# Performance work log

Measured on AMD Instinct MI355X. Metric: run time of the kernel, lower is better.

The kernel has to match this reference:

```python
import jax, jax.numpy as jnp
import numpy as np

N_NODES = 327680      # 8192 graphs * 40 nodes/graph
N_EDGES = 2621440     # avg degree 8
NODES_PER_GRAPH = 40


def _lin(k, fan_in, fan_out):
    s = 1.0 / np.sqrt(fan_in)
    return jax.random.uniform(k, (fan_in, fan_out), jnp.float32, -s, s)


def setup_inputs() -> dict:
    key = jax.random.key(0)
    ks = jax.random.split(key, 12)
    x = jax.random.normal(ks[0], (N_NODES, 58), jnp.float32)
    edge_index = jax.random.randint(ks[1], (2, N_EDGES), 0, N_NODES, dtype=jnp.int32)
    return {
        "x": x,
        "edge_index": edge_index,
        "W1": _lin(ks[2], 58, 96),  "b1": jnp.zeros((96,), jnp.float32),
        "W2": _lin(ks[3], 96, 48),  "b2": jnp.zeros((48,), jnp.float32),
        "l1_w": _lin(ks[4], 40 * 48, 256), "l1_b": jnp.zeros((256,), jnp.float32),
        "l2_w": _lin(ks[5], 256, 64),      "l2_b": jnp.zeros((64,), jnp.float32),
        "l3_w": _lin(ks[6], 64, 1),        "l3_b": jnp.zeros((1,), jnp.float32),
    }


def gcn_conv(x, src, dst, W, b, n):
    # PyG GCNConv: h = X W; out[i] = sum_{(j->i)} d_j^-1/2 d_i^-1/2 h[j] + b
    h = x @ W                                   # [N, out]
    deg = jnp.zeros((n,), h.dtype).at[dst].add(1.0)
    dinv = jnp.where(deg > 0, jax.lax.rsqrt(deg), 0.0)
    norm = dinv[src] * dinv[dst]                # [E]
    out = jax.ops.segment_sum(h[src] * norm[:, None], dst, num_segments=n)
    return out + b


def reference(x, edge_index, W1, b1, W2, b2, l1_w, l1_b, l2_w, l2_b, l3_w, l3_b):
    n = x.shape[0]
    loop = jnp.arange(n, dtype=edge_index.dtype)        # self-loops (PyG default)
    src = jnp.concatenate([edge_index[0], loop])
    dst = jnp.concatenate([edge_index[1], loop])
    h = jax.nn.relu(gcn_conv(x, src, dst, W1, b1, n))   # dropout is identity in eval
    h = jax.nn.relu(gcn_conv(h, src, dst, W2, b2, n))
    g = h.reshape(n // NODES_PER_GRAPH, NODES_PER_GRAPH * 48)
    g = jax.nn.relu(g @ l1_w + l1_b)
    g = jax.nn.relu(g @ l2_w + l2_b)
    return jax.nn.sigmoid(g @ l3_w + l3_b)              # [B, 1]
```

## Files before the change

### kernel.cpp

```cpp
#include <hip/hip_runtime.h>

#define N_NODES 327680
#define N_EDGES 2621440
#define NGRAPH  8192
#define NB      640
#define BCAPE   4608

typedef unsigned int uint;
typedef unsigned short u16;
typedef __attribute__((ext_vector_type(8))) short s16x8;
typedef __attribute__((ext_vector_type(4))) float f32x4;

__device__ __forceinline__ float b2f(u16 h){ return __uint_as_float(((uint)h)<<16); }
__device__ __forceinline__ u16 f2b(float f){
    uint u = __float_as_uint(f);
    u += 0x7fffu + ((u>>16)&1u);
    return (u16)(u>>16);
}


__global__ void k_initgcur(int* __restrict__ gcur){
    int i = blockIdx.x*256 + threadIdx.x;
    if (i < NB) gcur[i] = i*BCAPE;
}


__global__ __launch_bounds__(256) void k_partition(
    const int* __restrict__ src, const int* __restrict__ dst,
    int* __restrict__ gcur, uint2* __restrict__ staging)
{
    __shared__ int cnt[NB], base_[NB];
    int tid = threadIdx.x;
    for (int i = tid; i < NB; i += 256) cnt[i] = 0;
    __syncthreads();
    int e0 = blockIdx.x*4096;
    int d[16];
    #pragma unroll
    for (int j = 0; j < 16; ++j){
        d[j] = dst[e0 + j*256 + tid];
        atomicAdd(&cnt[d[j] >> 9], 1);
    }
    __syncthreads();
    for (int i = tid; i < NB; i += 256)
        base_[i] = atomicAdd(&gcur[i], cnt[i]);
    __syncthreads();
    for (int i = tid; i < NB; i += 256) cnt[i] = 0;
    __syncthreads();
    #pragma unroll
    for (int j = 0; j < 16; ++j){
        int e = e0 + j*256 + tid;
        int b = d[j] >> 9;
        int r = atomicAdd(&cnt[b], 1);
        staging[base_[b] + r] = make_uint2((uint)src[e], (uint)d[j]);
    }
}


__global__ __launch_bounds__(512) void k_bucket(
    const uint2* __restrict__ staging, const int* __restrict__ gcur,
    int* __restrict__ rowst, int* __restrict__ rendg, float* __restrict__ dinvg,
    int* __restrict__ csr, int* __restrict__ perm)
{
    __shared__ uint2 sedge[BCAPE];
    __shared__ int deg[512];
    __shared__ int sc[512];
    __shared__ int cur[512];
    __shared__ int dh[64], dbase[64];
    const int b = blockIdx.x;
    const int tid = threadIdx.x;
    const int lo = b*BCAPE;
    int cnt = gcur[b] - lo;
    if (cnt > BCAPE) cnt = BCAPE;
    deg[tid] = 0;
    if (tid < 64) dh[tid] = 0;
    __syncthreads();
    for (int t = tid; t < cnt; t += 512){
        uint2 ed = staging[lo + t];
        sedge[t] = ed;
        atomicAdd(&deg[ed.y & 511], 1);
    }
    __syncthreads();
    int d = deg[tid];
    sc[tid] = d;
    __syncthreads();
    for (int o = 1; o < 512; o <<= 1){
        int v = (tid >= o) ? sc[tid-o] : 0;
        __syncthreads();
        sc[tid] += v;
        __syncthreads();
    }
    int incl = sc[tid];
    int excl = incl - d;
    int gnode = b*512 + tid;
    rowst[gnode] = lo + excl;
    rendg[gnode] = lo + incl;
    dinvg[gnode] = 1.0f / sqrtf((float)(d + 1));
    cur[tid] = lo + excl;
    int bin = min(d, 63);
    atomicAdd(&dh[bin], 1);
    __syncthreads();
    if (tid == 0){
        int a = 0;
        #pragma unroll
        for (int i = 0; i < 64; ++i){ dbase[i] = a; a += dh[i]; dh[i] = 0; }
    }
    __syncthreads();
    int pos = dbase[bin] + atomicAdd(&dh[bin], 1);
    perm[b*512 + pos] = gnode;
    for (int t = tid; t < cnt; t += 512){
        uint2 ed = sedge[t];
        int p = atomicAdd(&cur[ed.y & 511], 1);
        csr[p] = (int)ed.x;
    }
}


__global__ __launch_bounds__(256) void k_trconv(const float* __restrict__ in, u16* __restrict__ out,
                                                int K, int N, int Kpad){
    __shared__ u16 t[64][72];
    int kb = blockIdx.x*64, nb = blockIdx.y*64;
    for (int i = threadIdx.x; i < 4096; i += 256){
        int k = i >> 6, n = i & 63;
        int gk = kb + k, gn = nb + n;
        float v = (gk < K && gn < N) ? in[(size_t)gk*N + gn] : 0.f;
        t[n][k] = f2b(v);
    }
    __syncthreads();
    for (int i = threadIdx.x; i < 4096; i += 256){
        int n = i >> 6, k = i & 63;
        int gk = kb + k, gn = nb + n;
        if (gn < N && gk < Kpad) out[(size_t)gn*Kpad + gk] = t[n][k];
    }
}


__global__ void k_prescale2(const float* __restrict__ x, const float* __restrict__ dinv,
                            uint* __restrict__ xs32){
    int gid = blockIdx.x*256 + threadIdx.x;
    int node = gid >> 5, c = gid & 31;
    float dv = dinv[node];
    float a = 0.f, b = 0.f;
    if (c < 29){
        float2 v = *(const float2*)&x[(size_t)node*58 + 2*c];
        a = v.x * dv; b = v.y * dv;
    }
    xs32[(size_t)node*32 + c] = (uint)f2b(a) | ((uint)f2b(b) << 16);
}


template<int BR>
__global__ __launch_bounds__(256) void k_gatherv(
    const int* __restrict__ rs, const int* __restrict__ re,
    const int* __restrict__ csr, const float* __restrict__ dinv,
    const int* __restrict__ perm,
    const uint2* __restrict__ feat2,
    const float* __restrict__ bias,
    u16* __restrict__ out)
{
    int slot = (blockIdx.x*256 + threadIdx.x) >> 4;
    int c2 = threadIdx.x & 15;
    int node = perm[slot];
    uint2 u = feat2[((uint)node << 4) + c2];
    float a0 = __uint_as_float(u.x << 16);
    float a1 = __uint_as_float(u.x & 0xffff0000u);
    float a2 = __uint_as_float(u.y << 16);
    float a3 = __uint_as_float(u.y & 0xffff0000u);
    int e = rs[node];
    const int e1 = re[node];
    if (e < e1){
        const int last = e1 - 1;
        int i0 = csr[e];
        int i1 = csr[min(e+1, last)];
        int i2 = csr[min(e+2, last)];
        int i3 = csr[min(e+3, last)];
        for (;;){
            int en = e + 4;
            bool more = en < e1;
            int j0=0, j1=0, j2=0, j3=0;
            if (more){
                j0 = csr[en];
                j1 = csr[min(en+1, last)];
                j2 = csr[min(en+2, last)];
                j3 = csr[min(en+3, last)];
            }
            uint2 u0 = feat2[((uint)i0 << 4) + c2];
            uint2 u1 = feat2[((uint)i1 << 4) + c2];
            uint2 u2 = feat2[((uint)i2 << 4) + c2];
            uint2 u3 = feat2[((uint)i3 << 4) + c2];
            if (e+1 >= e1){ u1.x = 0; u1.y = 0; }
            if (e+2 >= e1){ u2.x = 0; u2.y = 0; }
            if (e+3 >= e1){ u3.x = 0; u3.y = 0; }
            a0 += __uint_as_float(u0.x << 16); a1 += __uint_as_float(u0.x & 0xffff0000u);
            a2 += __uint_as_float(u0.y << 16); a3 += __uint_as_float(u0.y & 0xffff0000u);
            a0 += __uint_as_float(u1.x << 16); a1 += __uint_as_float(u1.x & 0xffff0000u);
            a2 += __uint_as_float(u1.y << 16); a3 += __uint_as_float(u1.y & 0xffff0000u);
            a0 += __uint_as_float(u2.x << 16); a1 += __uint_as_float(u2.x & 0xffff0000u);
            a2 += __uint_as_float(u2.y << 16); a3 += __uint_as_float(u2.y & 0xffff0000u);
            a0 += __uint_as_float(u3.x << 16); a1 += __uint_as_float(u3.x & 0xffff0000u);
            a2 += __uint_as_float(u3.y << 16); a3 += __uint_as_float(u3.y & 0xffff0000u);
            if (!more) break;
            i0 = j0; i1 = j1; i2 = j2; i3 = j3;
            e = en;
        }
    }
    float di = dinv[node];
    a0 *= di; a1 *= di; a2 *= di; a3 *= di;
    if (BR){
        if (c2 < 12){
            a0 = fmaxf(a0 + bias[4*c2+0], 0.f);
            a1 = fmaxf(a1 + bias[4*c2+1], 0.f);
            a2 = fmaxf(a2 + bias[4*c2+2], 0.f);
            a3 = fmaxf(a3 + bias[4*c2+3], 0.f);
            uint2 w;
            w.x = (uint)f2b(a0) | ((uint)f2b(a1) << 16);
            w.y = (uint)f2b(a2) | ((uint)f2b(a3) << 16);
            *(uint2*)&out[(size_t)node*48 + c2*4] = w;
        }
    } else {
        uint2 w;
        w.x = (uint)f2b(a0) | ((uint)f2b(a1) << 16);
        w.y = (uint)f2b(a2) | ((uint)f2b(a3) << 16);
        *(uint2*)&out[(size_t)node*64 + c2*4] = w;
    }
}


__global__ __launch_bounds__(256) void k_conv_mlp(
    const u16* __restrict__ A,
    const u16* __restrict__ w1t,
    const float* __restrict__ b1,
    const u16* __restrict__ w2t,
    const float* __restrict__ dinv,
    u16* __restrict__ ts)
{
    __shared__ __align__(16) u16 As[64][72];
    __shared__ __align__(16) u16 Bt1[96][72];
    __shared__ __align__(16) u16 Bt2[48][104];
    __shared__ __align__(16) u16 sh1[64][104];
    __shared__ float sb1[96];
    const int tid = threadIdx.x;
    {
        const u16* Ab = A + (size_t)blockIdx.x*64*64;
        for (int i = tid; i < 512; i += 256){
            int r = i >> 3, s = i & 7;
            *(uint4*)&As[r][s*8] = *(const uint4*)&Ab[r*64 + s*8];
        }
    }
    for (int i = tid; i < 768; i += 256){
        int n = i >> 3, s = i & 7;
        *(uint4*)&Bt1[n][s*8] = *(const uint4*)&w1t[n*64 + s*8];
    }
    for (int i = tid; i < 576; i += 256){
        int n = i / 12, s = i % 12;
        *(uint4*)&Bt2[n][s*8] = *(const uint4*)&w2t[n*96 + s*8];
    }
    if (tid < 96) sb1[tid] = b1[tid];
    __syncthreads();

    const int wv = tid >> 6, l = tid & 63;
    const int lr = l & 15, lg = l >> 4;
    const int r0 = wv*16;

    f32x4 acc1[6] = {};
    #pragma unroll
    for (int s = 0; s < 2; ++s){
        s16x8 af = *(const s16x8*)&As[r0+lr][s*32 + lg*8];
        #pragma unroll
        for (int t = 0; t < 6; ++t){
            s16x8 bf = *(const s16x8*)&Bt1[t*16+lr][s*32 + lg*8];
            acc1[t] = __builtin_amdgcn_mfma_f32_16x16x32_bf16(af, bf, acc1[t], 0, 0, 0);
        }
    }
    #pragma unroll
    for (int t = 0; t < 6; ++t){
        int col = t*16 + lr;
        float bias = sb1[col];
        #pragma unroll
        for (int r = 0; r < 4; ++r)
            sh1[r0 + lg*4 + r][col] = f2b(fmaxf(acc1[t][r] + bias, 0.f));
    }
    __syncthreads();

    f32x4 acc2[3] = {};
    #pragma unroll
    for (int s = 0; s < 3; ++s){
        s16x8 af = *(const s16x8*)&sh1[r0+lr][s*32 + lg*8];
        #pragma unroll
        for (int t = 0; t < 3; ++t){
            s16x8 bf = *(const s16x8*)&Bt2[t*16+lr][s*32 + lg*8];
            acc2[t] = __builtin_amdgcn_mfma_f32_16x16x32_bf16(af, bf, acc2[t], 0, 0, 0);
        }
    }
    size_t gbase = (size_t)blockIdx.x*64;
    #pragma unroll
    for (int r = 0; r < 4; ++r){
        size_t row = gbase + r0 + lg*4 + r;
        float dv = dinv[row];
        #pragma unroll
        for (int t = 0; t < 3; ++t)
            ts[row*64 + t*16 + lr] = f2b(acc2[t][r] * dv);
        ts[row*64 + 48 + lr] = 0;
    }
}


__global__ __launch_bounds__(256) void k_head(
    const u16* __restrict__ A,
    const u16* __restrict__ l1wt,
    const float* __restrict__ l1b,
    const u16* __restrict__ l2wt,
    const float* __restrict__ l2b,
    const float* __restrict__ l3w, const float* __restrict__ l3b,
    float* __restrict__ out)
{
    __shared__ __align__(16) u16 As[32][72];
    __shared__ __align__(16) u16 Bt[256][72];
    __shared__ float part[32][2];
    u16 (*sh1)[264] = (u16(*)[264])&Bt[0][0];
    const int tid = threadIdx.x;
    const int g0 = blockIdx.x*32;
    const int w = tid >> 6, l = tid & 63;
    const int lr = l & 15, lg = l >> 4;
    const int r0 = (w & 1)*16;
    const int c0 = (w >> 1)*128;
    f32x4 acc[8] = {};
    for (int k0 = 0; k0 < 1920; k0 += 64){
        __syncthreads();
        {
            int r = tid >> 3, s = tid & 7;
            *(uint4*)&As[r][s*8] = *(const uint4*)&A[(size_t)(g0+r)*1920 + k0 + s*8];
        }
        for (int i = tid; i < 2048; i += 256){
            int n = i >> 3, s = i & 7;
            *(uint4*)&Bt[n][s*8] = *(const uint4*)&l1wt[(size_t)n*1920 + k0 + s*8];
        }
        __syncthreads();
        #pragma unroll
        for (int s = 0; s < 2; ++s){
            s16x8 af = *(const s16x8*)&As[r0+lr][s*32 + lg*8];
            #pragma unroll
            for (int t = 0; t < 8; ++t){
                s16x8 bf = *(const s16x8*)&Bt[c0 + t*16 + lr][s*32 + lg*8];
                acc[t] = __builtin_amdgcn_mfma_f32_16x16x32_bf16(af, bf, acc[t], 0, 0, 0);
            }
        }
    }
    __syncthreads();
    #pragma unroll
    for (int t = 0; t < 8; ++t){
        int col = c0 + t*16 + lr;
        float bs = l1b[col];
        #pragma unroll
        for (int r = 0; r < 4; ++r)
            sh1[r0 + lg*4 + r][col] = f2b(fmaxf(acc[t][r] + bs, 0.f));
    }
    __syncthreads();
    f32x4 acc2[2] = {};
    #pragma unroll
    for (int s = 0; s < 8; ++s){
        s16x8 af = *(const s16x8*)&sh1[r0+lr][s*32 + lg*8];
        #pragma unroll
        for (int t = 0; t < 2; ++t){
            int col = (w>>1)*32 + t*16 + lr;
            s16x8 bf = *(const s16x8*)&l2wt[(size_t)col*256 + s*32 + lg*8];
            acc2[t] = __builtin_amdgcn_mfma_f32_16x16x32_bf16(af, bf, acc2[t], 0, 0, 0);
        }
    }
    float p[4];
    #pragma unroll
    for (int r = 0; r < 4; ++r){
        p[r] = 0.f;
        #pragma unroll
        for (int t = 0; t < 2; ++t){
            int col = (w>>1)*32 + t*16 + lr;
            p[r] += fmaxf(acc2[t][r] + l2b[col], 0.f) * l3w[col];
        }
    }
    #pragma unroll
    for (int o = 1; o < 16; o <<= 1){
        #pragma unroll
        for (int r = 0; r < 4; ++r) p[r] += __shfl_xor(p[r], o);
    }
    if (lr == 0){
        #pragma unroll
        for (int r = 0; r < 4; ++r)
            part[r0 + lg*4 + r][w>>1] = p[r];
    }
    __syncthreads();
    if (tid < 32)
        out[g0 + tid] = 1.0f / (1.0f + expf(-(part[tid][0] + part[tid][1] + l3b[0])));
}

extern "C" void kernel_launch(void* const* d_in, const int* in_sizes, int n_in,
                              void* d_out, int out_size, void* d_ws, size_t ws_size,
                              hipStream_t stream){
    const float* x   = (const float*)d_in[0];
    const int*   ei  = (const int*)  d_in[1];
    const int*   src = ei;
    const int*   dst = ei + N_EDGES;
    const float* W1  = (const float*)d_in[2];
    const float* b1  = (const float*)d_in[3];
    const float* W2  = (const float*)d_in[4];
    const float* b2  = (const float*)d_in[5];
    const float* l1w = (const float*)d_in[6];
    const float* l1b = (const float*)d_in[7];
    const float* l2w = (const float*)d_in[8];
    const float* l2b = (const float*)d_in[9];
    const float* l3w = (const float*)d_in[10];
    const float* l3b = (const float*)d_in[11];
    float* out = (float*)d_out;

    char* w = (char*)d_ws;
    auto alloc = [&](size_t bytes){ void* p = (void*)w; w += (bytes + 255) & ~(size_t)255; return p; };
    float* dinv   = (float*)alloc((size_t)N_NODES*4);
    int*   rowst  = (int*)  alloc((size_t)N_NODES*4);
    int*   rend   = (int*)  alloc((size_t)N_NODES*4);
    int*   perm   = (int*)  alloc((size_t)N_NODES*4);
    int*   gcur   = (int*)  alloc(NB*4);
    u16*   w1t    = (u16*)  alloc(96*64*2);
    u16*   w2t    = (u16*)  alloc(48*96*2);
    u16*   l1wt   = (u16*)  alloc((size_t)256*1920*2);
    u16*   l2wt   = (u16*)  alloc((size_t)64*256*2);
    int*   csr    = (int*)  alloc((size_t)NB*BCAPE*4);
    char*  BUF_A  = (char*) alloc((size_t)N_NODES*64*2);
    char*  BUF_B  = (char*) alloc((size_t)N_NODES*64*2);
    char*  BUF_C  = (char*) alloc((size_t)N_NODES*64*2);

    u16*   agg1    = (u16*)BUF_A;
    u16*   agg2    = (u16*)BUF_A;
    uint2* staging = (uint2*)BUF_B;
    uint*  xs32    = (uint*)BUF_B;
    u16*   ts      = (u16*)BUF_C;

    k_trconv<<<dim3(1,2),  256, 0, stream>>>(W1,  w1t,  58,   96,  64);
    k_trconv<<<dim3(2,1),  256, 0, stream>>>(W2,  w2t,  96,   48,  96);
    k_trconv<<<dim3(30,4), 256, 0, stream>>>(l1w, l1wt, 1920, 256, 1920);
    k_trconv<<<dim3(4,1),  256, 0, stream>>>(l2w, l2wt, 256,  64,  256);

    k_initgcur <<<3,   256, 0, stream>>>(gcur);
    k_partition<<<640, 256, 0, stream>>>(src, dst, gcur, staging);
    k_bucket   <<<640, 512, 0, stream>>>(staging, gcur, rowst, rend, dinv, csr, perm);

    k_prescale2  <<<40960, 256, 0, stream>>>(x, dinv, xs32);
    k_gatherv<0> <<<20480, 256, 0, stream>>>(rowst, rend, csr, dinv, perm,
                                             (const uint2*)xs32, nullptr, agg1);
    k_conv_mlp   <<<5120,  256, 0, stream>>>(agg1, w1t, b1, w2t, dinv, ts);

    k_gatherv<1> <<<20480, 256, 0, stream>>>(rowst, rend, csr, dinv, perm,
                                             (const uint2*)ts, b2, agg2);

    k_head       <<<256,   256, 0, stream>>>(agg2, l1wt, l1b, l2wt, l2b, l3w, l3b, out);
}
```

Baseline: 363.4 us.

## Widen gather to 16-byte loads, pack staging edges, merge prep kernels

The neighbor gather now has 8 lanes per node, each loading uint4 (8 bf16) instead of 16 lanes loading uint2, and it unrolls 8 edges per iteration with all index loads issued before the feature loads. Staging edges are packed into a single 32-bit word (19-bit src plus 9-bit local dst) instead of uint2, which halves partition/bucket traffic. The four weight-transpose launches and the gcur init are merged into one k_prep kernel to cut launch overhead. The wider per-thread loop raises register pressure and leaves fewer threads per node.

```diff
diff --git a/kernel.cpp b/kernel.cpp
--- a/kernel.cpp
+++ b/kernel.cpp
@@ -11,23 +11,55 @@
 typedef __attribute__((ext_vector_type(8))) short s16x8;
 typedef __attribute__((ext_vector_type(4))) float f32x4;
 
-__device__ __forceinline__ float b2f(u16 h){ return __uint_as_float(((uint)h)<<16); }
+__device__ __forceinline__ float bl(uint u){ return __uint_as_float(u << 16); }
+__device__ __forceinline__ float bh(uint u){ return __uint_as_float(u & 0xffff0000u); }
 __device__ __forceinline__ u16 f2b(float f){
     uint u = __float_as_uint(f);
     u += 0x7fffu + ((u>>16)&1u);
     return (u16)(u>>16);
 }
-
-
-__global__ void k_initgcur(int* __restrict__ gcur){
-    int i = blockIdx.x*256 + threadIdx.x;
-    if (i < NB) gcur[i] = i*BCAPE;
+__device__ __forceinline__ uint pk(float a, float b){
+    return (uint)f2b(a) | ((uint)f2b(b) << 16);
+}
+
+
+__device__ void tr_tile(const float* __restrict__ in, u16* __restrict__ out,
+                        int K, int N, int Kpad, int kb, int nb){
+    __shared__ u16 t[64][72];
+    for (int i = threadIdx.x; i < 4096; i += 256){
+        int k = i >> 6, n = i & 63;
+        int gk = kb + k, gn = nb + n;
+        float v = (gk < K && gn < N) ? in[(size_t)gk*N + gn] : 0.f;
+        t[n][k] = f2b(v);
+    }
+    __syncthreads();
+    for (int i = threadIdx.x; i < 4096; i += 256){
+        int n = i >> 6, k = i & 63;
+        int gk = kb + k, gn = nb + n;
+        if (gn < N && gk < Kpad) out[(size_t)gn*Kpad + gk] = t[n][k];
+    }
+}
+
+__global__ __launch_bounds__(256) void k_prep(
+    const float* __restrict__ W1, const float* __restrict__ W2,
+    const float* __restrict__ l1w, const float* __restrict__ l2w,
+    u16* __restrict__ w1t, u16* __restrict__ w2t,
+    u16* __restrict__ l1wt, u16* __restrict__ l2wt, int* __restrict__ gcur)
+{
+    int b = blockIdx.x;
+    if (b < 120)      tr_tile(l1w, l1wt, 1920, 256, 1920, (b%30)*64, (b/30)*64);
+    else if (b < 124) tr_tile(l2w, l2wt, 256,  64,  256,  (b-120)*64, 0);
+    else if (b < 126) tr_tile(W1,  w1t,  58,   96,  64,   0, (b-124)*64);
+    else if (b < 128) tr_tile(W2,  w2t,  96,   48,  96,   (b-126)*64, 0);
+    else {
+        for (int i = threadIdx.x; i < NB; i += 256) gcur[i] = 0;
+    }
 }
 
 
 __global__ __launch_bounds__(256) void k_partition(
     const int* __restrict__ src, const int* __restrict__ dst,
-    int* __restrict__ gcur, uint2* __restrict__ staging)
+    int* __restrict__ gcur, uint* __restrict__ staging)
 {
     __shared__ int cnt[NB], base_[NB];
     int tid = threadIdx.x;
@@ -51,17 +83,17 @@
         int e = e0 + j*256 + tid;
         int b = d[j] >> 9;
         int r = atomicAdd(&cnt[b], 1);
-        staging[base_[b] + r] = make_uint2((uint)src[e], (uint)d[j]);
+        staging[(uint)b*BCAPE + base_[b] + r] = (uint)src[e] | ((uint)(d[j] & 511) << 19);
     }
 }
 
 
 __global__ __launch_bounds__(512) void k_bucket(
-    const uint2* __restrict__ staging, const int* __restrict__ gcur,
+    const uint* __restrict__ staging, const int* __restrict__ gcur,
     int* __restrict__ rowst, int* __restrict__ rendg, float* __restrict__ dinvg,
     int* __restrict__ csr, int* __restrict__ perm)
 {
-    __shared__ uint2 sedge[BCAPE];
+    __shared__ uint sedge[BCAPE];
     __shared__ int deg[512];
     __shared__ int sc[512];
     __shared__ int cur[512];
@@ -69,15 +101,15 @@
     const int b = blockIdx.x;
     const int tid = threadIdx.x;
     const int lo = b*BCAPE;
-    int cnt = gcur[b] - lo;
+    int cnt = gcur[b];
     if (cnt > BCAPE) cnt = BCAPE;
     deg[tid] = 0;
     if (tid < 64) dh[tid] = 0;
     __syncthreads();
     for (int t = tid; t < cnt; t += 512){
-        uint2 ed = staging[lo + t];
+        uint ed = staging[lo + t];
         sedge[t] = ed;
-        atomicAdd(&deg[ed.y & 511], 1);
+        atomicAdd(&deg[ed >> 19], 1);
     }
     __syncthreads();
     int d = deg[tid];
@@ -108,28 +140,9 @@
     int pos = dbase[bin] + atomicAdd(&dh[bin], 1);
     perm[b*512 + pos] = gnode;
     for (int t = tid; t < cnt; t += 512){
-        uint2 ed = sedge[t];
-        int p = atomicAdd(&cur[ed.y & 511], 1);
-        csr[p] = (int)ed.x;
-    }
-}
-
-
-__global__ __launch_bounds__(256) void k_trconv(const float* __restrict__ in, u16* __restrict__ out,
-                                                int K, int N, int Kpad){
-    __shared__ u16 t[64][72];
-    int kb = blockIdx.x*64, nb = blockIdx.y*64;
-    for (int i = threadIdx.x; i < 4096; i += 256){
-        int k = i >> 6, n = i & 63;
-        int gk = kb + k, gn = nb + n;
-        float v = (gk < K && gn < N) ? in[(size_t)gk*N + gn] : 0.f;
-        t[n][k] = f2b(v);
-    }
-    __syncthreads();
-    for (int i = threadIdx.x; i < 4096; i += 256){
-        int n = i >> 6, k = i & 63;
-        int gk = kb + k, gn = nb + n;
-        if (gn < N && gk < Kpad) out[(size_t)gn*Kpad + gk] = t[n][k];
+        uint ed = sedge[t];
+        int p = atomicAdd(&cur[ed >> 19], 1);
+        csr[p] = (int)(ed & 0x7FFFFu);
     }
 }
 
@@ -144,7 +157,7 @@
         float2 v = *(const float2*)&x[(size_t)node*58 + 2*c];
         a = v.x * dv; b = v.y * dv;
     }
-    xs32[(size_t)node*32 + c] = (uint)f2b(a) | ((uint)f2b(b) << 16);
+    xs32[(size_t)node*32 + c] = pk(a, b);
 }
 
 
@@ -153,74 +166,56 @@
     const int* __restrict__ rs, const int* __restrict__ re,
     const int* __restrict__ csr, const float* __restrict__ dinv,
     const int* __restrict__ perm,
-    const uint2* __restrict__ feat2,
+    const uint4* __restrict__ feat4,
     const float* __restrict__ bias,
     u16* __restrict__ out)
 {
-    int slot = (blockIdx.x*256 + threadIdx.x) >> 4;
-    int c2 = threadIdx.x & 15;
+    int slot = (blockIdx.x*256 + threadIdx.x) >> 3;
+    int c4 = threadIdx.x & 7;
     int node = perm[slot];
-    uint2 u = feat2[((uint)node << 4) + c2];
-    float a0 = __uint_as_float(u.x << 16);
-    float a1 = __uint_as_float(u.x & 0xffff0000u);
-    float a2 = __uint_as_float(u.y << 16);
-    float a3 = __uint_as_float(u.y & 0xffff0000u);
+    uint4 u = feat4[((uint)node << 3) + c4];
+    float a0 = bl(u.x), a1 = bh(u.x), a2 = bl(u.y), a3 = bh(u.y);
+    float a4 = bl(u.z), a5 = bh(u.z), a6 = bl(u.w), a7 = bh(u.w);
     int e = rs[node];
     const int e1 = re[node];
-    if (e < e1){
+    while (e < e1){
         const int last = e1 - 1;
-        int i0 = csr[e];
-        int i1 = csr[min(e+1, last)];
-        int i2 = csr[min(e+2, last)];
-        int i3 = csr[min(e+3, last)];
-        for (;;){
-            int en = e + 4;
-            bool more = en < e1;
-            int j0=0, j1=0, j2=0, j3=0;
-            if (more){
-                j0 = csr[en];
-                j1 = csr[min(en+1, last)];
-                j2 = csr[min(en+2, last)];
-                j3 = csr[min(en+3, last)];
+        int idx[8];
+        #pragma unroll
+        for (int k = 0; k < 8; ++k) idx[k] = csr[min(e + k, last)];
+        uint4 uu[8];
+        #pragma unroll
+        for (int k = 0; k < 8; ++k) uu[k] = feat4[((uint)idx[k] << 3) + c4];
+        #pragma unroll
+        for (int k = 0; k < 8; ++k){
+            if (e + k < e1){
+                a0 += bl(uu[k].x); a1 += bh(uu[k].x);
+                a2 += bl(uu[k].y); a3 += bh(uu[k].y);
+                a4 += bl(uu[k].z); a5 += bh(uu[k].z);
+                a6 += bl(uu[k].w); a7 += bh(uu[k].w);
             }
-            uint2 u0 = feat2[((uint)i0 << 4) + c2];
-            uint2 u1 = feat2[((uint)i1 << 4) + c2];
-            uint2 u2 = feat2[((uint)i2 << 4) + c2];
-            uint2 u3 = feat2[((uint)i3 << 4) + c2];
-            if (e+1 >= e1){ u1.x = 0; u1.y = 0; }
-            if (e+2 >= e1){ u2.x = 0; u2.y = 0; }
-            if (e+3 >= e1){ u3.x = 0; u3.y = 0; }
-            a0 += __uint_as_float(u0.x << 16); a1 += __uint_as_float(u0.x & 0xffff0000u);
-            a2 += __uint_as_float(u0.y << 16); a3 += __uint_as_float(u0.y & 0xffff0000u);
-            a0 += __uint_as_float(u1.x << 16); a1 += __uint_as_float(u1.x & 0xffff0000u);
-            a2 += __uint_as_float(u1.y << 16); a3 += __uint_as_float(u1.y & 0xffff0000u);
-            a0 += __uint_as_float(u2.x << 16); a1 += __uint_as_float(u2.x & 0xffff0000u);
-            a2 += __uint_as_float(u2.y << 16); a3 += __uint_as_float(u2.y & 0xffff0000u);
-            a0 += __uint_as_float(u3.x << 16); a1 += __uint_as_float(u3.x & 0xffff0000u);
-            a2 += __uint_as_float(u3.y << 16); a3 += __uint_as_float(u3.y & 0xffff0000u);
-            if (!more) break;
-            i0 = j0; i1 = j1; i2 = j2; i3 = j3;
-            e = en;
-        }
+        }
+        e += 8;
     }
     float di = dinv[node];
     a0 *= di; a1 *= di; a2 *= di; a3 *= di;
+    a4 *= di; a5 *= di; a6 *= di; a7 *= di;
     if (BR){
-        if (c2 < 12){
-            a0 = fmaxf(a0 + bias[4*c2+0], 0.f);
-            a1 = fmaxf(a1 + bias[4*c2+1], 0.f);
-            a2 = fmaxf(a2 + bias[4*c2+2], 0.f);
-            a3 = fmaxf(a3 + bias[4*c2+3], 0.f);
-            uint2 w;
-            w.x = (uint)f2b(a0) | ((uint)f2b(a1) << 16);
-            w.y = (uint)f2b(a2) | ((uint)f2b(a3) << 16);
-            *(uint2*)&out[(size_t)node*48 + c2*4] = w;
+        if (c4 < 6){
+            float4 bz0 = *(const float4*)&bias[8*c4];
+            float4 bz1 = *(const float4*)&bias[8*c4 + 4];
+            a0 = fmaxf(a0 + bz0.x, 0.f); a1 = fmaxf(a1 + bz0.y, 0.f);
+            a2 = fmaxf(a2 + bz0.z, 0.f); a3 = fmaxf(a3 + bz0.w, 0.f);
+            a4 = fmaxf(a4 + bz1.x, 0.f); a5 = fmaxf(a5 + bz1.y, 0.f);
+            a6 = fmaxf(a6 + bz1.z, 0.f); a7 = fmaxf(a7 + bz1.w, 0.f);
+            uint4 w;
+            w.x = pk(a0,a1); w.y = pk(a2,a3); w.z = pk(a4,a5); w.w = pk(a6,a7);
+            *(uint4*)&out[(size_t)node*48 + c4*8] = w;
         }
     } else {
-        uint2 w;
-        w.x = (uint)f2b(a0) | ((uint)f2b(a1) << 16);
-        w.y = (uint)f2b(a2) | ((uint)f2b(a3) << 16);
-        *(uint2*)&out[(size_t)node*64 + c2*4] = w;
+        uint4 w;
+        w.x = pk(a0,a1); w.y = pk(a2,a3); w.z = pk(a4,a5); w.w = pk(a6,a7);
+        *(uint4*)&out[(size_t)node*64 + c4*8] = w;
     }
 }
 
@@ -428,26 +423,22 @@
 
     u16*   agg1    = (u16*)BUF_A;
     u16*   agg2    = (u16*)BUF_A;
-    uint2* staging = (uint2*)BUF_B;
+    uint*  staging = (uint*)BUF_B;
     uint*  xs32    = (uint*)BUF_B;
     u16*   ts      = (u16*)BUF_C;
 
-    k_trconv<<<dim3(1,2),  256, 0, stream>>>(W1,  w1t,  58,   96,  64);
-    k_trconv<<<dim3(2,1),  256, 0, stream>>>(W2,  w2t,  96,   48,  96);
-    k_trconv<<<dim3(30,4), 256, 0, stream>>>(l1w, l1wt, 1920, 256, 1920);
-    k_trconv<<<dim3(4,1),  256, 0, stream>>>(l2w, l2wt, 256,  64,  256);
-
-    k_initgcur <<<3,   256, 0, stream>>>(gcur);
+    k_prep     <<<129, 256, 0, stream>>>(W1, W2, l1w, l2w, w1t, w2t, l1wt, l2wt, gcur);
+
     k_partition<<<640, 256, 0, stream>>>(src, dst, gcur, staging);
     k_bucket   <<<640, 512, 0, stream>>>(staging, gcur, rowst, rend, dinv, csr, perm);
 
     k_prescale2  <<<40960, 256, 0, stream>>>(x, dinv, xs32);
-    k_gatherv<0> <<<20480, 256, 0, stream>>>(rowst, rend, csr, dinv, perm,
-                                             (const uint2*)xs32, nullptr, agg1);
+    k_gatherv<0> <<<10240, 256, 0, stream>>>(rowst, rend, csr, dinv, perm,
+                                             (const uint4*)xs32, nullptr, agg1);
     k_conv_mlp   <<<5120,  256, 0, stream>>>(agg1, w1t, b1, w2t, dinv, ts);
 
-    k_gatherv<1> <<<20480, 256, 0, stream>>>(rowst, rend, csr, dinv, perm,
-                                             (const uint2*)ts, b2, agg2);
+    k_gatherv<1> <<<10240, 256, 0, stream>>>(rowst, rend, csr, dinv, perm,
+                                             (const uint4*)ts, b2, agg2);
 
     k_head       <<<256,   256, 0, stream>>>(agg2, l1wt, l1b, l2wt, l2b, l3w, l3b, out);
 }
```

Result: faster. 341.3 us (-6.1%).
